# Kernel optimization log

Measured on AMD Instinct MI355X. Metric: run time of the kernel, lower is better.

Reference implementation:

```python
import jax, jax.numpy as jnp
import numpy as np

B, C, N, K = 2, 128, 8192, 16
DL = 128  # dim_L; Fourier half-dim = 64; mlp hidden = 32


def setup_inputs() -> dict:
    key = jax.random.key(0)
    ks = jax.random.split(key, 16)
    s = 0.05
    return {
        "x": jax.random.normal(ks[0], (B, C, N, 1), jnp.float32),
        "coords": jax.random.normal(ks[1], (B, N, 4), jnp.float32),
        "idx": jax.random.randint(ks[2], (B, N, K), 0, N, jnp.int64),
        "B_gauss": jax.random.normal(ks[3], (4, DL // 2), jnp.float32),
        "W1": jax.random.normal(ks[4], (DL, DL // 4), jnp.float32) * s,
        "b1": jax.random.normal(ks[5], (DL // 4,), jnp.float32) * s,
        "W2": jax.random.normal(ks[6], (DL // 4, C), jnp.float32) * s,
        "b2": jax.random.normal(ks[7], (C,), jnp.float32) * s,
        "Wq": jax.random.normal(ks[8], (C, C), jnp.float32) * s,
        "bq": jax.random.normal(ks[9], (C,), jnp.float32) * s,
        "Wk": jax.random.normal(ks[10], (C, C), jnp.float32) * s,
        "bk": jax.random.normal(ks[11], (C,), jnp.float32) * s,
        "Wv": jax.random.normal(ks[12], (C, C), jnp.float32) * s,
        "bv": jax.random.normal(ks[13], (C,), jnp.float32) * s,
        "Wo": jax.random.normal(ks[14], (C, C), jnp.float32) * s,
        "bo": jax.random.normal(ks[15], (C,), jnp.float32) * s,
    }


def reference(x, coords, idx, B_gauss, W1, b1, W2, b2, Wq, bq, Wk, bk, Wv, bv, Wo, bo):
    xs = x[..., 0]  # [B, C, N]
    # gather neighbor coords/features via KNN idx (vmapped over batch)
    nb_coords = jax.vmap(lambda c, i: c[i])(coords, idx)          # [B, N, K, 4]
    nb_feats = jax.vmap(lambda f, i: f[:, i])(xs, idx)            # [B, C, N, K]
    delta_p = nb_coords - coords[:, :, None, :]                   # [B, N, K, 4]
    # random-Fourier geometric embedding
    proj = jnp.matmul(delta_p, B_gauss)                           # [B, N, K, DL/2]
    two_pi = 2.0 * jnp.pi
    E_freq = jnp.concatenate([jnp.sin(two_pi * proj), jnp.cos(two_pi * proj)], axis=-1)
    h = jax.nn.relu(E_freq @ W1 + b1) @ W2 + b2                   # [B, N, K, C]
    E_geo = jnp.transpose(h, (0, 3, 1, 2))                        # [B, C, N, K]
    # 1x1 conv projections == channel matmuls (PyTorch conv weight acts as out<-in)
    Q = jnp.einsum('oc,bcn->bon', Wq, xs) + bq[None, :, None]     # [B, C, N]
    KV_in = nb_feats + E_geo                                      # [B, C, N, K]
    Kt = jnp.einsum('oc,bcnk->bonk', Wk, KV_in) + bk[None, :, None, None]
    Vt = jnp.einsum('oc,bcnk->bonk', Wv, KV_in) + bv[None, :, None, None]
    # local dot-product attention over K neighbors
    attn = jnp.sum(Q[..., None] * Kt, axis=1, keepdims=True) / jnp.sqrt(jnp.float32(C))
    attn = jax.nn.softmax(attn, axis=-1)                          # [B, 1, N, K]
    out = jnp.sum(attn * Vt, axis=-1, keepdims=True)              # [B, C, N, 1]
    out = jnp.einsum('oc,bcnk->bonk', Wo, out) + bo[None, :, None, None]
    return out
```

## Files before the change

kernel.cpp:

```cpp
#include <hip/hip_runtime.h>


using u16 = unsigned short;
using u32 = unsigned int;
using u64 = unsigned long long;

typedef short bf16x8 __attribute__((ext_vector_type(8)));
typedef float f32x4  __attribute__((ext_vector_type(4)));

__device__ __forceinline__ float bl(u32 u) { return __uint_as_float(u << 16); }
__device__ __forceinline__ float bh(u32 u) { return __uint_as_float(u & 0xffff0000u); }
__device__ __forceinline__ float b2f(u16 u) { return __uint_as_float(((u32)u) << 16); }
__device__ __forceinline__ u16 f2b(float f) {
    u32 u = __float_as_uint(f);
    u32 r = u + 0x7fffu + ((u >> 16) & 1u);
    return (u16)(r >> 16);
}
__device__ __forceinline__ u64 pack4(float a, float b, float c, float d) {
    return (u64)f2b(a) | ((u64)f2b(b) << 16) | ((u64)f2b(c) << 32) | ((u64)f2b(d) << 48);
}
__device__ __forceinline__ int fidxA(int m, int c) {
    return (((m >> 4)*4 + (c >> 5))*64 + ((c >> 3) & 3)*16 + (m & 15))*8 + (c & 7);
}

__global__ void __launch_bounds__(512)
k_pt(const float* __restrict__ x,
     const float* __restrict__ Wq, const float* __restrict__ bq,
     const float* __restrict__ Wk,
     const float* __restrict__ Wv, const float* __restrict__ bv,
     const float* __restrict__ Wo, const float* __restrict__ bo,
     const float* __restrict__ W1, const float* __restrict__ W2,
     u16* __restrict__ Afrag, u16* __restrict__ Wovfrag,
     u16* __restrict__ W1frag, u16* __restrict__ W2frag,
     u16* __restrict__ Wow2frag,
     float* __restrict__ bA, float* __restrict__ bov,
     u16* __restrict__ xT)
{
    const int blk = blockIdx.x, tid = threadIdx.x;

    if (blk >= 130) {
        __shared__ u16 tile[32][33];
        const int blk2 = blk - 130;
        const int b  = blk2 >> 10;
        const int ct = (blk2 >> 8) & 3;
        const int nt = blk2 & 255;
        const int tx = tid & 31, ty = tid >> 5;
        const size_t xb = (size_t)b * 128 * 8192;
        #pragma unroll
        for (int j = 0; j < 2; ++j) {
            int c = ct*32 + ty + j*16;
            tile[ty + j*16][tx] = f2b(x[xb + (size_t)c * 8192 + (size_t)(nt*32 + tx)]);
        }
        __syncthreads();
        #pragma unroll
        for (int j = 0; j < 2; ++j) {
            int n = nt*32 + ty + j*16;
            xT[xb + (size_t)n * 128 + (size_t)(ct*32 + tx)] = tile[tx][ty + j*16];
        }
        return;
    }

    const int i = tid & 127, p = tid >> 7;
    if (blk < 128) {
        __shared__ float sWk[128], sWo[128];
        __shared__ float s_pA[4][128], s_pV[4][128];
        __shared__ float sWovRow[128];
        __shared__ float s_p2[32][17];
        if (tid < 128) sWk[tid] = Wk[tid*128 + blk];
        else if (tid < 256) sWo[tid-128] = Wo[blk*128 + (tid-128)];
        __syncthreads();
        float accA = 0.f, accV = 0.f;
        #pragma unroll 8
        for (int o = p*32; o < p*32 + 32; ++o) {
            accA += sWk[o] * Wq[o*128 + i];
            accV += sWo[o] * Wv[o*128 + i];
        }
        s_pA[p][i] = accA; s_pV[p][i] = accV;
        __syncthreads();
        if (tid < 128) {
            float v = s_pA[0][tid] + s_pA[1][tid] + s_pA[2][tid] + s_pA[3][tid];
            Afrag[fidxA(blk, tid)] = f2b(v);
        } else if (tid < 256) {
            int ii = tid - 128;
            float v = s_pV[0][ii] + s_pV[1][ii] + s_pV[2][ii] + s_pV[3][ii];
            Wovfrag[fidxA(blk, ii)] = f2b(v);
            sWovRow[ii] = v;
        }
        __syncthreads();
        {
            int h = tid >> 4, sub = tid & 15;
            float a = 0.f;
            #pragma unroll
            for (int jj = 0; jj < 8; ++jj)
                a += sWovRow[sub*8 + jj] * W2[h*128 + sub*8 + jj];
            s_p2[h][sub] = a;
        }
        __syncthreads();
        if (tid < 32) {
            float v = 0.f;
            #pragma unroll
            for (int s = 0; s < 16; ++s) v += s_p2[tid][s];
            Wow2frag[(((blk >> 4)*64 + (tid >> 3)*16 + (blk & 15)))*8 + (tid & 7)] = f2b(v);
        }
    } else if (blk == 128) {
        __shared__ float s_r[2][4][128];
        float a1 = 0.f, a3 = 0.f;
        #pragma unroll 8
        for (int o = p*32; o < p*32 + 32; ++o) {
            a1 += Wk[o*128 + i] * bq[o];
            a3 += Wo[i*128 + o] * bv[o];
        }
        s_r[0][p][i] = a1; s_r[1][p][i] = a3;
        __syncthreads();
        if (tid < 128) {
            bA[tid] = s_r[0][0][tid] + s_r[0][1][tid] + s_r[0][2][tid] + s_r[0][3][tid];
        } else if (tid < 256) {
            int ii = tid - 128;
            bov[ii] = s_r[1][0][ii] + s_r[1][1][ii] + s_r[1][2][ii] + s_r[1][3][ii] + bo[ii];
        }
    } else {
        for (int e = tid; e < 4096; e += 512) {
            int ii = e & 127, r2 = e >> 7;
            {
                int nt = r2 >> 4, lmm = r2 & 15;
                int ks = ii >> 5, q = (ii >> 3) & 3, j = ii & 7;
                W1frag[((nt*4 + ks)*64 + q*16 + lmm)*8 + j] = f2b(W1[ii*32 + r2]);
            }
            {
                int mt = r2 >> 4, lmm = r2 & 15;
                int ks = ii >> 5, q = (ii >> 3) & 3, j = ii & 7;
                W2frag[((mt*4 + ks)*64 + q*16 + lmm)*8 + j] = f2b(W2[r2*128 + ii]);
            }
        }
    }
}

__global__ void __launch_bounds__(256, 2)
k_main(const u16* __restrict__ xT, const float* __restrict__ coords,
       const int* __restrict__ idx, const float* __restrict__ Bg,
       const float* __restrict__ b1g, const float* __restrict__ b2g,
       const u16* __restrict__ Afrag, const u16* __restrict__ Wovfrag,
       const u16* __restrict__ W1frag, const u16* __restrict__ W2frag,
       const u16* __restrict__ Wow2frag,
       const float* __restrict__ bAg, const float* __restrict__ bovg,
       float* __restrict__ out)
{
    __shared__ __align__(16) u16   sH[256][40];
    __shared__ __align__(16) u16   s_qkb[16][136];
    __shared__ __align__(16) u16   s_gb[16][40];
    __shared__ __align__(16) u16   s_xbb[16][136];
    __shared__ __align__(16) float s_del[256][4];
    __shared__ float s_attn[16][17];
    __shared__ u16   sHbar[32][18];
    __shared__ __align__(16) float s_b2[128];
    __shared__ float s_bov[128], s_b1[32];
    __shared__ __align__(16) float sBgT[64][4];
    __shared__ int s_idx[256];

    const int tid = threadIdx.x;
    const int w = tid >> 6, l = tid & 63, lm = l & 15, lq = l >> 4;
    const int g0 = blockIdx.x * 16;
    const int bsel = g0 >> 13;
    const int n0 = g0 & 8191;
    const size_t bbase = ((size_t)bsel) << 13;
    const float inv_sqrtC = 0.08838834764831845f;

    if (tid < 128) { s_bov[tid] = bovg[tid]; s_b2[tid] = b2g[tid]; }
    else if (tid < 160) { s_b1[tid-128] = b1g[tid-128]; }
    sBgT[tid >> 2][tid & 3] = Bg[(tid & 3)*64 + (tid >> 2)];

    {
        int j = idx[(size_t)g0*16 + tid];
        s_idx[tid] = j;
        float4 cj = *(const float4*)&coords[(size_t)(bbase + j)*4];
        float4 cn = *(const float4*)&coords[(size_t)(g0 + (tid >> 4))*4];
        *(float4*)s_del[tid] = make_float4(cj.x-cn.x, cj.y-cn.y, cj.z-cn.z, cj.w-cn.w);
    }
    {
        f32x4 accq[2] = {{0.f,0.f,0.f,0.f},{0.f,0.f,0.f,0.f}};
        const bf16x8* Af = (const bf16x8*)Afrag;
        bf16x8 bfr[4];
        #pragma unroll
        for (int ks = 0; ks < 4; ++ks)
            bfr[ks] = *(const bf16x8*)&xT[(((size_t)(g0 + lm)) << 7) + ks*32 + lq*8];
        #pragma unroll
        for (int mi = 0; mi < 2; ++mi) {
            const int ct = w*2 + mi;
            #pragma unroll
            for (int ks = 0; ks < 4; ++ks) {
                bf16x8 a = Af[(ct*4 + ks)*64 + l];
                accq[mi] = __builtin_amdgcn_mfma_f32_16x16x32_bf16(a, bfr[ks], accq[mi], 0, 0, 0);
            }
        }
        #pragma unroll
        for (int mi = 0; mi < 2; ++mi) {
            int c0 = (w*2 + mi)*16 + lq*4;
            float4 ba4 = *(const float4*)&bAg[c0];
            *(u64*)&s_qkb[lm][c0] = pack4(accq[mi][0] + ba4.x, accq[mi][1] + ba4.y,
                                          accq[mi][2] + ba4.z, accq[mi][3] + ba4.w);
        }
    }
    __syncthreads();

    {
        const bf16x8* W1f = (const bf16x8*)W1frag;
        bf16x8 w1f[2][4];
        #pragma unroll
        for (int nt = 0; nt < 2; ++nt)
            #pragma unroll
            for (int ks = 0; ks < 4; ++ks) w1f[nt][ks] = W1f[(nt*4 + ks)*64 + l];
        #pragma unroll
        for (int mi = 0; mi < 4; ++mi) {
            const int mt = w*4 + mi;
            float4 d = *(const float4*)s_del[mt*16 + lm];
            bf16x8 ea[4];
            #pragma unroll
            for (int ksp = 0; ksp < 2; ++ksp) {
                #pragma unroll
                for (int jp = 0; jp < 4; ++jp) {
                    int f = ksp*32 + lq*8 + jp*2;
                    float4 ga = *(const float4*)sBgT[f];
                    float4 gb = *(const float4*)sBgT[f+1];
                    float p0 = d.x*ga.x + d.y*ga.y + d.z*ga.z + d.w*ga.w;
                    float p1 = d.x*gb.x + d.y*gb.y + d.z*gb.z + d.w*gb.w;
                    p0 -= floorf(p0); p1 -= floorf(p1);
                    ((u32*)&ea[ksp])[jp]   = (u32)f2b(__builtin_amdgcn_sinf(p0))
                                           | ((u32)f2b(__builtin_amdgcn_sinf(p1)) << 16);
                    ((u32*)&ea[ksp+2])[jp] = (u32)f2b(__builtin_amdgcn_cosf(p0))
                                           | ((u32)f2b(__builtin_amdgcn_cosf(p1)) << 16);
                }
            }
            f32x4 acch[2] = {{0.f,0.f,0.f,0.f},{0.f,0.f,0.f,0.f}};
            #pragma unroll
            for (int ks = 0; ks < 4; ++ks) {
                acch[0] = __builtin_amdgcn_mfma_f32_16x16x32_bf16(ea[ks], w1f[0][ks], acch[0], 0,0,0);
                acch[1] = __builtin_amdgcn_mfma_f32_16x16x32_bf16(ea[ks], w1f[1][ks], acch[1], 0,0,0);
            }
            #pragma unroll
            for (int nt = 0; nt < 2; ++nt) {
                float b1v = s_b1[nt*16 + lm];
                #pragma unroll
                for (int r = 0; r < 4; ++r)
                    sH[mt*16 + lq*4 + r][nt*16 + lm] = f2b(fmaxf(acch[nt][r] + b1v, 0.f));
            }
        }
    }
    if (w < 2) {
        const bf16x8* W2f = (const bf16x8*)W2frag;
        f32x4 accg = {0.f,0.f,0.f,0.f};
        #pragma unroll
        for (int ks = 0; ks < 4; ++ks) {
            bf16x8 a = W2f[(w*4 + ks)*64 + l];
            bf16x8 bv = *(const bf16x8*)&s_qkb[lm][ks*32 + lq*8];
            accg = __builtin_amdgcn_mfma_f32_16x16x32_bf16(a, bv, accg, 0, 0, 0);
        }
        {
            int m0 = w*16 + lq*4;
            *(u64*)&s_gb[lm][m0] = pack4(accg[0], accg[1], accg[2], accg[3]);
        }
    }
    __syncthreads();

    {
        bf16x8 bq4[5];
        #pragma unroll
        for (int ks = 0; ks < 4; ++ks) bq4[ks] = *(const bf16x8*)&s_qkb[lm][ks*32 + lq*8];
        bq4[4] = *(const bf16x8*)&s_gb[lm][lq*8];
        #pragma unroll
        for (int mi = 0; mi < 4; ++mi) {
            const int mt = w*4 + mi;
            bf16x8 xnb[4];
            const size_t rb = ((size_t)(bbase + s_idx[mt*16 + lm])) << 7;
            #pragma unroll
            for (int ks = 0; ks < 4; ++ks)
                xnb[ks] = *(const bf16x8*)&xT[rb + ks*32 + lq*8];
            f32x4 acc = {0.f,0.f,0.f,0.f};
            #pragma unroll
            for (int ks = 0; ks < 4; ++ks)
                acc = __builtin_amdgcn_mfma_f32_16x16x32_bf16(xnb[ks], bq4[ks], acc, 0, 0, 0);
            {
                bf16x8 a = *(const bf16x8*)&sH[mt*16 + lm][lq*8];
                acc = __builtin_amdgcn_mfma_f32_16x16x32_bf16(a, bq4[4], acc, 0, 0, 0);
            }
            float s0 = acc[0]*inv_sqrtC, s1 = acc[1]*inv_sqrtC;
            float s2 = acc[2]*inv_sqrtC, s3 = acc[3]*inv_sqrtC;
            float mx = fmaxf(fmaxf(s0, s1), fmaxf(s2, s3));
            mx = fmaxf(mx, __shfl_xor(mx, 16));
            mx = fmaxf(mx, __shfl_xor(mx, 32));
            float e0 = __expf(s0 - mx), e1 = __expf(s1 - mx);
            float e2 = __expf(s2 - mx), e3 = __expf(s3 - mx);
            float sm = (e0 + e1) + (e2 + e3);
            sm += __shfl_xor(sm, 16);
            sm += __shfl_xor(sm, 32);
            if (lm == mt) {
                float inv = 1.0f / sm;
                s_attn[mt][lq*4 + 0] = e0*inv;
                s_attn[mt][lq*4 + 1] = e1*inv;
                s_attn[mt][lq*4 + 2] = e2*inv;
                s_attn[mt][lq*4 + 3] = e3*inv;
            }
        }
    }
    __syncthreads();

    {
        int n = tid >> 4, cs = tid & 15, c0 = cs*8;
        float a0[16];
        #pragma unroll
        for (int k = 0; k < 16; ++k) a0[k] = s_attn[n][k];
        float4 f0 = *(const float4*)&s_b2[c0];
        float4 f1 = *(const float4*)&s_b2[c0+4];
        #pragma unroll
        for (int k = 0; k < 16; ++k) {
            uint4 v = *(const uint4*)&xT[(((size_t)(bbase + s_idx[n*16 + k])) << 7) + c0];
            f0.x += a0[k]*bl(v.x); f0.y += a0[k]*bh(v.x);
            f0.z += a0[k]*bl(v.y); f0.w += a0[k]*bh(v.y);
            f1.x += a0[k]*bl(v.z); f1.y += a0[k]*bh(v.z);
            f1.z += a0[k]*bl(v.w); f1.w += a0[k]*bh(v.w);
        }
        *(u64*)&s_xbb[n][c0]   = pack4(f0.x, f0.y, f0.z, f0.w);
        *(u64*)&s_xbb[n][c0+4] = pack4(f1.x, f1.y, f1.z, f1.w);
        int m0 = cs*2;
        float h0 = 0.f, h1 = 0.f;
        #pragma unroll
        for (int k = 0; k < 16; ++k) {
            float ak = a0[k];
            u32 hv = *(const u32*)&sH[n*16 + k][m0];
            h0 += ak * bl(hv);
            h1 += ak * bh(hv);
        }
        sHbar[m0][n]   = f2b(h0);
        sHbar[m0+1][n] = f2b(h1);
    }
    __syncthreads();

    {
        const bf16x8* Wvf = (const bf16x8*)Wovfrag;
        const bf16x8* W2f = (const bf16x8*)Wow2frag;
        bf16x8 bv[4];
        #pragma unroll
        for (int ks = 0; ks < 4; ++ks) bv[ks] = *(const bf16x8*)&s_xbb[lm][ks*32 + lq*8];
        bf16x8 bvh;
        #pragma unroll
        for (int j = 0; j < 8; ++j) bvh[j] = (short)sHbar[lq*8 + j][lm];
        #pragma unroll
        for (int mi = 0; mi < 2; ++mi) {
            const int ct = w*2 + mi;
            f32x4 acco = {0.f,0.f,0.f,0.f};
            acco = __builtin_amdgcn_mfma_f32_16x16x32_bf16(W2f[ct*64 + l], bvh, acco, 0, 0, 0);
            #pragma unroll
            for (int ks = 0; ks < 4; ++ks) {
                bf16x8 a = Wvf[(ct*4 + ks)*64 + l];
                acco = __builtin_amdgcn_mfma_f32_16x16x32_bf16(a, bv[ks], acco, 0, 0, 0);
            }
            #pragma unroll
            for (int r = 0; r < 4; ++r) {
                int o = ct*16 + lq*4 + r;
                out[(((size_t)(bsel*128 + o)) << 13) + n0 + lm] = acco[r] + s_bov[o];
            }
        }
    }
}

extern "C" void kernel_launch(void* const* d_in, const int* in_sizes, int n_in,
                              void* d_out, int out_size, void* d_ws, size_t ws_size,
                              hipStream_t stream)
{
    const float* x      = (const float*)d_in[0];
    const float* coords = (const float*)d_in[1];
    const int*   idx    = (const int*)d_in[2];
    const float* Bg     = (const float*)d_in[3];
    const float* W1     = (const float*)d_in[4];
    const float* b1     = (const float*)d_in[5];
    const float* W2     = (const float*)d_in[6];
    const float* b2     = (const float*)d_in[7];
    const float* Wq     = (const float*)d_in[8];
    const float* bq     = (const float*)d_in[9];
    const float* Wk     = (const float*)d_in[10];
    const float* bk     = (const float*)d_in[11];
    const float* Wv     = (const float*)d_in[12];
    const float* bv     = (const float*)d_in[13];
    const float* Wo     = (const float*)d_in[14];
    const float* bo     = (const float*)d_in[15];
    float* out = (float*)d_out;
    (void)bk;

    char* ws = (char*)d_ws;
    u16*   Afrag    = (u16*)(ws);
    u16*   Wovfrag  = (u16*)(ws + 32768);
    u16*   W1frag   = (u16*)(ws + 65536);
    u16*   W2frag   = (u16*)(ws + 73728);
    u16*   Wow2frag = (u16*)(ws + 81920);
    float* bA       = (float*)(ws + 90112);
    float* bov      = (float*)(ws + 90624);
    u16*   xT       = (u16*)(ws + 94208);

    k_pt<<<2178, 512, 0, stream>>>(x, Wq, bq, Wk, Wv, bv, Wo, bo, W1, W2,
                                   Afrag, Wovfrag, W1frag, W2frag, Wow2frag,
                                   bA, bov, xT);
    k_main<<<1024, 256, 0, stream>>>(xT, coords, idx, Bg, b1, b2,
                                     Afrag, Wovfrag, W1frag, W2frag, Wow2frag,
                                     bA, bov, out);
}
```

Measured before the change: 123.6 us.

## Precompute per-point Fourier sin/cos and use angle-difference identity for neighbors

```diff
diff --git a/kernel.cpp b/kernel.cpp
--- a/kernel.cpp
+++ b/kernel.cpp
@@ -10,21 +10,24 @@
 
 __device__ __forceinline__ float bl(u32 u) { return __uint_as_float(u << 16); }
 __device__ __forceinline__ float bh(u32 u) { return __uint_as_float(u & 0xffff0000u); }
-__device__ __forceinline__ float b2f(u16 u) { return __uint_as_float(((u32)u) << 16); }
 __device__ __forceinline__ u16 f2b(float f) {
     u32 u = __float_as_uint(f);
     u32 r = u + 0x7fffu + ((u >> 16) & 1u);
     return (u16)(r >> 16);
 }
+__device__ __forceinline__ u32 pk2(float lo, float hi) {
+    return (u32)f2b(lo) | ((u32)f2b(hi) << 16);
+}
 __device__ __forceinline__ u64 pack4(float a, float b, float c, float d) {
-    return (u64)f2b(a) | ((u64)f2b(b) << 16) | ((u64)f2b(c) << 32) | ((u64)f2b(d) << 48);
+    return (u64)pk2(a, b) | ((u64)pk2(c, d) << 32);
 }
 __device__ __forceinline__ int fidxA(int m, int c) {
     return (((m >> 4)*4 + (c >> 5))*64 + ((c >> 3) & 3)*16 + (m & 15))*8 + (c & 7);
 }
 
 __global__ void __launch_bounds__(512)
-k_pt(const float* __restrict__ x,
+k_pt(const float* __restrict__ x, const float* __restrict__ coords,
+     const float* __restrict__ Bg,
      const float* __restrict__ Wq, const float* __restrict__ bq,
      const float* __restrict__ Wk,
      const float* __restrict__ Wv, const float* __restrict__ bv,
@@ -34,9 +37,30 @@
      u16* __restrict__ W1frag, u16* __restrict__ W2frag,
      u16* __restrict__ Wow2frag,
      float* __restrict__ bA, float* __restrict__ bov,
-     u16* __restrict__ xT)
+     u16* __restrict__ xT, u32* __restrict__ scT)
 {
     const int blk = blockIdx.x, tid = threadIdx.x;
+
+    if (blk >= 2178) {
+        __shared__ float sBg[64][4];
+        if (tid < 256) sBg[tid >> 2][tid & 3] = Bg[(tid & 3)*64 + (tid >> 2)];
+        __syncthreads();
+        const int p  = (blk - 2178)*64 + (tid >> 3);
+        const int f0 = (tid & 7)*8;
+        float4 c = *(const float4*)&coords[(size_t)p*4];
+        u32 ov[8];
+        #pragma unroll
+        for (int j = 0; j < 8; ++j) {
+            float4 g = *(const float4*)sBg[f0 + j];
+            float ph = c.x*g.x + c.y*g.y + c.z*g.z + c.w*g.w;
+            ph -= floorf(ph);
+            ov[j] = pk2(__builtin_amdgcn_sinf(ph), __builtin_amdgcn_cosf(ph));
+        }
+        u32* dst = &scT[(size_t)p*64 + f0];
+        *(uint4*)dst       = make_uint4(ov[0], ov[1], ov[2], ov[3]);
+        *(uint4*)(dst + 4) = make_uint4(ov[4], ov[5], ov[6], ov[7]);
+        return;
+    }
 
     if (blk >= 130) {
         __shared__ u16 tile[32][33];
@@ -136,8 +160,8 @@
 }
 
 __global__ void __launch_bounds__(256, 2)
-k_main(const u16* __restrict__ xT, const float* __restrict__ coords,
-       const int* __restrict__ idx, const float* __restrict__ Bg,
+k_main(const u16* __restrict__ xT, const u32* __restrict__ scT,
+       const int* __restrict__ idx,
        const float* __restrict__ b1g, const float* __restrict__ b2g,
        const u16* __restrict__ Afrag, const u16* __restrict__ Wovfrag,
        const u16* __restrict__ W1frag, const u16* __restrict__ W2frag,
@@ -149,12 +173,11 @@
     __shared__ __align__(16) u16   s_qkb[16][136];
     __shared__ __align__(16) u16   s_gb[16][40];
     __shared__ __align__(16) u16   s_xbb[16][136];
-    __shared__ __align__(16) float s_del[256][4];
+    __shared__ __align__(16) u32   s_scn[16][64];
     __shared__ float s_attn[16][17];
     __shared__ u16   sHbar[32][18];
     __shared__ __align__(16) float s_b2[128];
     __shared__ float s_bov[128], s_b1[32];
-    __shared__ __align__(16) float sBgT[64][4];
     __shared__ int s_idx[256];
 
     const int tid = threadIdx.x;
@@ -167,15 +190,12 @@
 
     if (tid < 128) { s_bov[tid] = bovg[tid]; s_b2[tid] = b2g[tid]; }
     else if (tid < 160) { s_b1[tid-128] = b1g[tid-128]; }
-    sBgT[tid >> 2][tid & 3] = Bg[(tid & 3)*64 + (tid >> 2)];
-
-    {
-        int j = idx[(size_t)g0*16 + tid];
-        s_idx[tid] = j;
-        float4 cj = *(const float4*)&coords[(size_t)(bbase + j)*4];
-        float4 cn = *(const float4*)&coords[(size_t)(g0 + (tid >> 4))*4];
-        *(float4*)s_del[tid] = make_float4(cj.x-cn.x, cj.y-cn.y, cj.z-cn.z, cj.w-cn.w);
-    }
+
+    *(uint4*)&s_scn[tid >> 4][(tid & 15)*4] =
+        *(const uint4*)&scT[(size_t)(g0 + (tid >> 4))*64 + (tid & 15)*4];
+
+    s_idx[tid] = idx[(size_t)g0*16 + tid];
+
     {
         f32x4 accq[2] = {{0.f,0.f,0.f,0.f},{0.f,0.f,0.f,0.f}};
         const bf16x8* Af = (const bf16x8*)Afrag;
@@ -212,22 +232,31 @@
         #pragma unroll
         for (int mi = 0; mi < 4; ++mi) {
             const int mt = w*4 + mi;
-            float4 d = *(const float4*)s_del[mt*16 + lm];
+            const int j = s_idx[mt*16 + lm];
+            const u32* scj = &scT[(size_t)(bbase + j)*64];
+            union { uint4 q[4]; u32 u[16]; } J, N;
+            J.q[0] = *(const uint4*)&scj[lq*8];
+            J.q[1] = *(const uint4*)&scj[lq*8 + 4];
+            J.q[2] = *(const uint4*)&scj[32 + lq*8];
+            J.q[3] = *(const uint4*)&scj[32 + lq*8 + 4];
+            N.q[0] = *(const uint4*)&s_scn[mt][lq*8];
+            N.q[1] = *(const uint4*)&s_scn[mt][lq*8 + 4];
+            N.q[2] = *(const uint4*)&s_scn[mt][32 + lq*8];
+            N.q[3] = *(const uint4*)&s_scn[mt][32 + lq*8 + 4];
             bf16x8 ea[4];
             #pragma unroll
             for (int ksp = 0; ksp < 2; ++ksp) {
                 #pragma unroll
                 for (int jp = 0; jp < 4; ++jp) {
-                    int f = ksp*32 + lq*8 + jp*2;
-                    float4 ga = *(const float4*)sBgT[f];
-                    float4 gb = *(const float4*)sBgT[f+1];
-                    float p0 = d.x*ga.x + d.y*ga.y + d.z*ga.z + d.w*ga.w;
-                    float p1 = d.x*gb.x + d.y*gb.y + d.z*gb.z + d.w*gb.w;
-                    p0 -= floorf(p0); p1 -= floorf(p1);
-                    ((u32*)&ea[ksp])[jp]   = (u32)f2b(__builtin_amdgcn_sinf(p0))
-                                           | ((u32)f2b(__builtin_amdgcn_sinf(p1)) << 16);
-                    ((u32*)&ea[ksp+2])[jp] = (u32)f2b(__builtin_amdgcn_cosf(p0))
-                                           | ((u32)f2b(__builtin_amdgcn_cosf(p1)) << 16);
+                    int t0 = ksp*8 + jp*2;
+                    u32 j0 = J.u[t0], j1 = J.u[t0+1];
+                    u32 n0u = N.u[t0], n1u = N.u[t0+1];
+                    float sj0 = bl(j0), cj0 = bh(j0), sn0 = bl(n0u), cn0 = bh(n0u);
+                    float sj1 = bl(j1), cj1 = bh(j1), sn1 = bl(n1u), cn1 = bh(n1u);
+                    float sv0 = sj0*cn0 - cj0*sn0, cv0 = cj0*cn0 + sj0*sn0;
+                    float sv1 = sj1*cn1 - cj1*sn1, cv1 = cj1*cn1 + sj1*sn1;
+                    ((u32*)&ea[ksp])[jp]   = pk2(sv0, sv1);
+                    ((u32*)&ea[ksp+2])[jp] = pk2(cv0, cv1);
                 }
             }
             f32x4 acch[2] = {{0.f,0.f,0.f,0.f},{0.f,0.f,0.f,0.f}};
@@ -394,11 +423,13 @@
     float* bA       = (float*)(ws + 90112);
     float* bov      = (float*)(ws + 90624);
     u16*   xT       = (u16*)(ws + 94208);
-
-    k_pt<<<2178, 512, 0, stream>>>(x, Wq, bq, Wk, Wv, bv, Wo, bo, W1, W2,
+    u32*   scT      = (u32*)(ws + 94208 + 4194304);
+
+    k_pt<<<2434, 512, 0, stream>>>(x, coords, Bg, Wq, bq, Wk, Wv, bv, Wo, bo,
+                                   W1, W2,
                                    Afrag, Wovfrag, W1frag, W2frag, Wow2frag,
-                                   bA, bov, xT);
-    k_main<<<1024, 256, 0, stream>>>(xT, coords, idx, Bg, b1, b2,
+                                   bA, bov, xT, scT);
+    k_main<<<1024, 256, 0, stream>>>(xT, scT, idx, b1, b2,
                                      Afrag, Wovfrag, W1frag, W2frag, Wow2frag,
                                      bA, bov, out);
 }
```

Measured after the change: 119.0 us, median of 2. 1.04x faster.
